# Kernel tuning notes

Hardware: AMD Instinct MI355X
Metric: run time of the kernel (lower is better)

The kernel has to match this reference:

```python
import jax, jax.numpy as jnp
import numpy as np

DIM = 1024
NUM_HEADS = 16
HEAD_DIM = DIM // NUM_HEADS
B, T = 2, 2048


def setup_inputs() -> dict:
    key = jax.random.key(0)
    ks = jax.random.split(key, 7)
    x = jax.random.normal(ks[0], (B, T, DIM), dtype=jnp.float32)
    # causal mask, broadcastable over batch and heads
    mask = jnp.tril(jnp.ones((T, T), dtype=bool))[None, None, :, :]
    # rope tables for half rotary angles, tiled to head_dim (cat of two halves)
    pos = jnp.arange(T, dtype=jnp.float32)[:, None]
    inv_freq = 1.0 / (10000.0 ** (jnp.arange(0, HEAD_DIM, 2, dtype=jnp.float32) / HEAD_DIM))
    ang = pos * inv_freq[None, :]                      # [T, hd/2]
    ang = jnp.concatenate([ang, ang], axis=-1)         # [T, hd]
    rope_sin = jnp.sin(ang)[None, None, :, :]
    rope_cos = jnp.cos(ang)[None, None, :, :]
    s = 0.02
    qkv_w = jax.random.normal(ks[1], (DIM, 3 * DIM), dtype=jnp.float32) * s
    qkv_b = jnp.zeros((3 * DIM,), dtype=jnp.float32)
    proj_w = jax.random.normal(ks[2], (DIM, DIM), dtype=jnp.float32) * s
    proj_b = jnp.zeros((DIM,), dtype=jnp.float32)
    return {"x": x, "mask": mask, "rope_sin": rope_sin, "rope_cos": rope_cos,
            "qkv_w": qkv_w, "qkv_b": qkv_b, "proj_w": proj_w, "proj_b": proj_b}


def _rotate_half(t):
    half = t.shape[-1] // 2
    return jnp.concatenate([-t[..., half:], t[..., :half]], axis=-1)


def _apply_rope(t, sin, cos):
    return t * cos + _rotate_half(t) * sin


def reference(x, mask, rope_sin, rope_cos, qkv_w, qkv_b, proj_w, proj_b):
    Bb, Tt, C = x.shape
    qkv = x @ qkv_w + qkv_b                            # [B, T, 3C]
    q, k, v = jnp.split(qkv, 3, axis=-1)
    def split_heads(t):                                # [B, T, C] -> [B, H, T, hd]
        return t.reshape(Bb, Tt, NUM_HEADS, HEAD_DIM).transpose(0, 2, 1, 3)
    q, k, v = split_heads(q), split_heads(k), split_heads(v)
    sin = rope_sin[:, :, :Tt, :]
    cos = rope_cos[:, :, :Tt, :]
    q = _apply_rope(q, sin, cos)
    k = _apply_rope(k, sin, cos)
    att = jnp.einsum("bhqd,bhkd->bhqk", q, k) / (HEAD_DIM ** 0.5)
    att = jnp.where(mask, att, -jnp.inf)
    att = jax.nn.softmax(att, axis=-1)
    y = jnp.einsum("bhqk,bhkd->bhqd", att, v)          # [B, H, T, hd]
    y = y.transpose(0, 2, 1, 3).reshape(Bb, Tt, C)
    return y @ proj_w + proj_b
```

## Files before the change

kernel.cpp:

```cpp
#include <hip/hip_runtime.h>

typedef unsigned short u16;
typedef u16 u16x8 __attribute__((ext_vector_type(8)));
typedef __bf16 bf16x8 __attribute__((ext_vector_type(8)));
typedef float f32x4 __attribute__((ext_vector_type(4)));

#define T_SEQ 2048
#define DIM 1024
#define NH 16
#define HD 64

#define MFMA(a, b, c) __builtin_amdgcn_mfma_f32_16x16x32_bf16(a, b, c, 0, 0, 0)

__device__ __forceinline__ u16 f2bf(float f) {
  return __builtin_bit_cast(u16, static_cast<__bf16>(f));
}

__device__ __forceinline__ bf16x8 ld8(const u16* p) {
  return __builtin_bit_cast(bf16x8, *(const u16x8*)p);
}

__device__ __forceinline__ void gload_lds16(const u16* g, u16* l) {
  __builtin_amdgcn_global_load_lds((const __attribute__((address_space(1))) void*)(g),
                                   (__attribute__((address_space(3))) void*)(l),
                                   16, 0, 0);
}

__global__ void k_prep(const float* __restrict__ X, u16* __restrict__ Y,
                       const float* __restrict__ Wq, u16* __restrict__ WqT,
                       const float* __restrict__ Wp, u16* __restrict__ WpT) {
  __shared__ float tile[32][33];
  int bid = blockIdx.x;
  if (bid < 4096) {
    int i = (bid * 256 + threadIdx.x) * 4;
    float4 f = *(const float4*)&X[i];
    ushort4 o = make_ushort4(f2bf(f.x), f2bf(f.y), f2bf(f.z), f2bf(f.w));
    *(ushort4*)&Y[i] = o;
    return;
  }
  const float* W; u16* WT; int K = 1024, N, bx, by;
  if (bid < 4096 + 3072) { int t = bid - 4096; W = Wq; WT = WqT; N = 3072; bx = t % 96; by = t / 96; }
  else                   { int t = bid - 7168; W = Wp; WT = WpT; N = 1024; bx = t % 32; by = t / 32; }
  int tx = threadIdx.x & 31, ty = threadIdx.x >> 5;
  int c0 = bx * 32, r0 = by * 32;
#pragma unroll
  for (int r = 0; r < 4; r++)
    tile[ty + r * 8][tx] = W[(r0 + ty + r * 8) * N + c0 + tx];
  __syncthreads();
#pragma unroll
  for (int r = 0; r < 4; r++)
    WT[(c0 + ty + r * 8) * K + r0 + tx] = f2bf(tile[tx][ty + r * 8]);
}


#define GEMM_STAGE3(buf, kk)                                                      \
  {                                                                               \
    _Pragma("unroll") for (int p = 0; p < 2; p++) {                               \
      int rr = w * 32 + p * 16;                                                   \
      gload_lds16(&Agp[(size_t)(rowBase + rr + srow) * Kd + (kk) + schunk],       \
                  &As[buf][rr * 32]);                                             \
      gload_lds16(&Bgp[(size_t)(colBase + rr + srow) * Kd + (kk) + schunk],       \
                  &Bs[buf][rr * 32]);                                             \
    }                                                                             \
  }

#define GEMM_COMPUTE3(buf)                                                        \
  {                                                                               \
    bf16x8 af[4], bfv[4];                                                         \
    _Pragma("unroll") for (int i = 0; i < 4; i++) {                               \
      af[i] = ld8(&As[buf][(wm * 64 + i * 16 + l15) * 32 + quad * 8]);            \
      bfv[i] = ld8(&Bs[buf][(wn * 64 + i * 16 + l15) * 32 + quad * 8]);           \
    }                                                                             \
    _Pragma("unroll") for (int i = 0; i < 4; i++)                                 \
        _Pragma("unroll") for (int j = 0; j < 4; j++)                             \
            acc[i][j] = MFMA(af[i], bfv[j], acc[i][j]);                           \
  }

#define GEMM_CORE3(Aptr, BTptr, bxv, byv)                                         \
  const int tid = threadIdx.x;                                                    \
  const int lane = tid & 63, w = tid >> 6;                                        \
  const int l15 = lane & 15, quad = lane >> 4;                                    \
  const int wm = w >> 1, wn = w & 1;                                              \
  const int rowBase = (byv) * 128;                                                \
  const int colBase = (bxv) * 128;                                                \
  const u16* Agp = (Aptr);                                                        \
  const u16* Bgp = (BTptr);                                                       \
  const int Kd = DIM;                                                             \
  f32x4 acc[4][4];                                                                \
  _Pragma("unroll") for (int i = 0; i < 4; i++)                                   \
      _Pragma("unroll") for (int j = 0; j < 4; j++)                               \
          acc[i][j] = (f32x4){0.f, 0.f, 0.f, 0.f};                                \
  const int srow = lane >> 2;                 \
  const int schunk = (lane & 3) * 8;    \
  GEMM_STAGE3(0, 0)                                                               \
  GEMM_STAGE3(1, 32)                                                              \
  _Pragma("unroll") for (int s = 0; s < 32; ++s) {                                \
    if (s < 31) { asm volatile("s_waitcnt vmcnt(4)" ::: "memory"); }              \
    else        { asm volatile("s_waitcnt vmcnt(0)" ::: "memory"); }              \
    __builtin_amdgcn_s_barrier();                                                 \
    if (s + 2 < 32) { GEMM_STAGE3((s + 2) % 3, (s + 2) * 32) }                    \
    GEMM_COMPUTE3(s % 3)                                                          \
  }                                                                               \
  __syncthreads();

#define EPLD 136

__global__ __launch_bounds__(256) void k_gemm_qkv(
    const u16* __restrict__ A, const u16* __restrict__ BT,
    const float* __restrict__ bias,
    const float* __restrict__ rsin, const float* __restrict__ rcos,
    u16* __restrict__ qb, u16* __restrict__ kb, u16* __restrict__ vtb) {
  __shared__ __align__(16) u16 LDSBUF[24576];
  u16 (*As)[128 * 32] = (u16(*)[128 * 32])(LDSBUF);
  u16 (*Bs)[128 * 32] = (u16(*)[128 * 32])(LDSBUF + 12288);
  const int n = blockIdx.x, xcd = n & 7, s = n >> 3;
  const int cg = xcd & 1, rg = xcd >> 1;
  const int bxv = cg * 12 + (s >> 3);
  const int byv = rg * 8 + (s & 7);
  GEMM_CORE3(A, BT, bxv, byv)

#pragma unroll
  for (int j = 0; j < 4; j++) {
    float bv = bias[colBase + wn * 64 + j * 16 + l15];
#pragma unroll
    for (int i = 0; i < 4; i++)
#pragma unroll
      for (int r = 0; r < 4; r++) acc[i][j][r] += bv;
  }

  const int colW = colBase + wn * 64;
  const int sec = colW >> 10;

  if (sec == 2) {
#pragma unroll
    for (int i = 0; i < 4; i++)
#pragma unroll
      for (int r = 0; r < 4; r++) {
        int tl = wm * 64 + i * 16 + quad * 4 + r;
#pragma unroll
        for (int j = 0; j < 4; j++) {
          int d2 = wn * 64 + j * 16 + l15;
          LDSBUF[d2 * EPLD + tl] = f2bf(acc[i][j][r]);
        }
      }
  } else {
#pragma unroll
    for (int i = 0; i < 4; i++)
#pragma unroll
      for (int r = 0; r < 4; r++) {
        int tl = wm * 64 + i * 16 + quad * 4 + r;
        int t = (rowBase + tl) & 2047;
#pragma unroll
        for (int j = 0; j < 4; j++) {
          int d = j * 16 + l15;
          float v = acc[i][j][r];
          float pr = acc[i][j ^ 2][r];
          float rot = (j < 2) ? -pr : pr;
          float rv = v * rcos[t * HD + d] + rot * rsin[t * HD + d];
          if (sec == 0) rv *= 0.125f;
          LDSBUF[tl * EPLD + wn * 64 + d] = f2bf(rv);
        }
      }
  }
  __syncthreads();

  const int hb = (colBase & 1023) >> 6;
  const int b = rowBase >> 11, t0 = rowBase & 2047;
  if (sec == 2) {
#pragma unroll
    for (int p = 0; p < 8; p++) {
      int drow = (tid >> 4) + p * 16;
      int tc = (tid & 15) * 8;
      int hh = hb + (drow >> 6), d = drow & 63;
      u16x8 v = *(const u16x8*)&LDSBUF[drow * EPLD + tc];
      *(u16x8*)&vtb[((size_t)(b * NH + hh) * HD + d) * T_SEQ + t0 + tc] = v;
    }
  } else {
    u16* dst = (sec == 0) ? qb : kb;
#pragma unroll
    for (int p = 0; p < 8; p++) {
      int row = (tid >> 4) + p * 16;
      int dc = (tid & 15) * 8;
      int hh = hb + (dc >> 6), d = dc & 63;
      u16x8 v = *(const u16x8*)&LDSBUF[row * EPLD + dc];
      *(u16x8*)&dst[((size_t)(b * NH + hh) * T_SEQ + t0 + row) * HD + d] = v;
    }
  }
}

__global__ __launch_bounds__(256) void k_gemm_proj(
    const u16* __restrict__ A, const u16* __restrict__ BT,
    const float* __restrict__ bias, float* __restrict__ C) {
  __shared__ __align__(16) u16 LDSBUF[24576];
  u16 (*As)[128 * 32] = (u16(*)[128 * 32])(LDSBUF);
  u16 (*Bs)[128 * 32] = (u16(*)[128 * 32])(LDSBUF + 12288);
  const int n = blockIdx.x, xcd = n & 7, s = n >> 3;
  const int cg = xcd & 1, rg = xcd >> 1;
  const int bxv = cg * 4 + (s >> 3);
  const int byv = rg * 8 + (s & 7);
  GEMM_CORE3(A, BT, bxv, byv)

#pragma unroll
  for (int i = 0; i < 4; i++)
#pragma unroll
    for (int r = 0; r < 4; r++) {
      int grow = rowBase + wm * 64 + i * 16 + quad * 4 + r;
#pragma unroll
      for (int j = 0; j < 4; j++) {
        int col = colBase + wn * 64 + j * 16 + l15;
        C[grow * DIM + col] = acc[i][j][r] + bias[col];
      }
    }
}

#define KLD 72
#define VLD 136

__global__ __launch_bounds__(256, 3) void k_attn(
    const u16* __restrict__ qb, const u16* __restrict__ kb,
    const u16* __restrict__ vtb, u16* __restrict__ yb) {
  __shared__ __align__(16) u16 Ks[128 * KLD];
  __shared__ __align__(16) u16 VTs[64 * VLD];
  __shared__ __align__(16) u16 Ps[64 * VLD];
  const int tid = threadIdx.x;
  const int lane = tid & 63, w = tid >> 6;
  const int l15 = lane & 15, quad = lane >> 4;
  const int bh = blockIdx.x;
  const int qt = 31 - blockIdx.y;

  const u16* qp = qb + (size_t)bh * T_SEQ * HD;
  const u16* kp = kb + (size_t)bh * T_SEQ * HD;
  const u16* vp = vtb + (size_t)bh * HD * T_SEQ;

  const int nch = (qt + 2) >> 1;
  const int qrow_base = qt * 64 + w * 16 + quad * 4;

  const int sr = tid >> 3, sc = (tid & 7) * 8;
  const int vr = tid >> 4, vc = (tid & 15) * 8;

  u16x8 kreg[4], vreg[4];
#define LOADKV(c)                                                              \
  {                                                                            \
    _Pragma("unroll") for (int p = 0; p < 4; p++)                              \
        kreg[p] = *(const u16x8*)&kp[((c) * 128 + sr + p * 32) * HD + sc];     \
    _Pragma("unroll") for (int p = 0; p < 4; p++)                              \
        vreg[p] = *(const u16x8*)&vp[(vr + p * 16) * T_SEQ + (c) * 128 + vc];  \
  }
#define WRITEK()                                                               \
  {                                                                            \
    _Pragma("unroll") for (int p = 0; p < 4; p++)                              \
        *(u16x8*)&Ks[(sr + p * 32) * KLD + sc] = kreg[p];                      \
  }
#define WRITEV()                                                               \
  {                                                                            \
    _Pragma("unroll") for (int p = 0; p < 4; p++)                              \
        *(u16x8*)&VTs[(vr + p * 16) * VLD + vc] = vreg[p];                     \
  }

  LOADKV(0)

  {
#pragma unroll
    for (int p = 0; p < 2; p++) {
      int r = sr + p * 32;
      *(u16x8*)&Ps[r * KLD + sc] = *(const u16x8*)&qp[(qt * 64 + r) * HD + sc];
    }
  }
  __syncthreads();
  bf16x8 qa0 = ld8(&Ps[(w * 16 + l15) * KLD + quad * 8]);
  bf16x8 qa1 = ld8(&Ps[(w * 16 + l15) * KLD + 32 + quad * 8]);
  WRITEK()
  WRITEV()
  __syncthreads();

  f32x4 o[4];
#pragma unroll
  for (int j = 0; j < 4; j++) o[j] = (f32x4){0.f, 0.f, 0.f, 0.f};
  float li[4] = {0.f, 0.f, 0.f, 0.f};

  u16* ps = &Ps[w * 16 * VLD];
  const int srd = ((l15 & 1) << 3) | ((l15 >> 2) << 1) | ((l15 >> 1) & 1);

  for (int c = 0; c < nch; c++) {
    const bool more = (c + 1 < nch);
    if (more) LOADKV(c + 1)

    f32x4 s[8];
#pragma unroll
    for (int j = 0; j < 8; j++) {
      s[j] = (f32x4){0.f, 0.f, 0.f, 0.f};
      bf16x8 b0 = ld8(&Ks[(j * 16 + l15) * KLD + quad * 8]);
      bf16x8 b1 = ld8(&Ks[(j * 16 + l15) * KLD + 32 + quad * 8]);
      s[j] = MFMA(qa0, b0, s[j]);
      s[j] = MFMA(qa1, b1, s[j]);
    }

    if (more) {
      asm volatile("s_waitcnt lgkmcnt(0)" ::: "memory");
      __builtin_amdgcn_s_barrier();
      __builtin_amdgcn_sched_barrier(0);
      WRITEK()
    }

    const bool lastc = (c == nch - 1);
#pragma unroll
    for (int r = 0; r < 4; r++) {
      const int swr = ((r & 1) << 3) | (quad << 1) | (r >> 1);
#pragma unroll
      for (int j = 0; j < 8; j++) {
        float e = __expf(s[j][r]);
        if (lastc && (c * 128 + j * 16 + l15 > qrow_base + r)) e = 0.f;
        li[r] += e;
        ps[swr * VLD + j * 16 + l15] = f2bf(e);
      }
    }

#pragma unroll
    for (int c4 = 0; c4 < 4; c4++) {
      bf16x8 pa = ld8(&ps[srd * VLD + c4 * 32 + quad * 8]);
#pragma unroll
      for (int j2 = 0; j2 < 4; j2++) {
        bf16x8 vb = ld8(&VTs[(j2 * 16 + l15) * VLD + c4 * 32 + quad * 8]);
        o[j2] = MFMA(pa, vb, o[j2]);
      }
    }

    if (more) {
      __syncthreads();
      WRITEV()
    }
  }

#pragma unroll
  for (int r = 0; r < 4; r++) {
#pragma unroll
    for (int off = 8; off >= 1; off >>= 1) li[r] += __shfl_xor(li[r], off, 16);
    li[r] = 1.0f / li[r];
  }

#pragma unroll
  for (int j = 0; j < 4; j++)
#pragma unroll
    for (int r = 0; r < 4; r++) {
      const int swr = ((r & 1) << 3) | (quad << 1) | (r >> 1);
      ps[swr * VLD + j * 16 + l15] = f2bf(o[j][r] * li[r]);
    }
  __syncthreads();

  const int b = bh >> 4, h = bh & 15;
  {
    int sr2 = tid >> 3, sc2 = (tid & 7) * 8;
#pragma unroll
    for (int p = 0; p < 2; p++) {
      int row = sr2 + p * 32;
      int m = row & 15;
      int srow = ((m & 1) << 3) | ((m >> 2) << 1) | ((m >> 1) & 1);
      int t = qt * 64 + row;
      *(u16x8*)&yb[((size_t)(b * T_SEQ + t) * NH + h) * HD + sc2] =
          *(const u16x8*)&Ps[((row & 48) | srow) * VLD + sc2];
    }
  }
}

extern "C" void kernel_launch(void* const* d_in, const int* in_sizes, int n_in,
                              void* d_out, int out_size, void* d_ws, size_t ws_size,
                              hipStream_t stream) {
  const float* x      = (const float*)d_in[0];
  const float* rsin   = (const float*)d_in[2];
  const float* rcos   = (const float*)d_in[3];
  const float* qkv_w  = (const float*)d_in[4];
  const float* qkv_b  = (const float*)d_in[5];
  const float* proj_w = (const float*)d_in[6];
  const float* proj_b = (const float*)d_in[7];
  float* out = (float*)d_out;

  char* ws = (char*)d_ws;
  u16* x_bf  = (u16*)(ws);
  u16* qkvT  = (u16*)(ws + (8ull << 20));
  u16* projT = (u16*)(ws + (14ull << 20));
  u16* q_buf = (u16*)(ws + (16ull << 20));
  u16* k_buf = (u16*)(ws + (24ull << 20));
  u16* vT    = (u16*)(ws + (32ull << 20));
  u16* y_buf = (u16*)(ws + (40ull << 20));

  hipLaunchKernelGGL(k_prep, dim3(8192), dim3(256), 0, stream,
                     x, x_bf, qkv_w, qkvT, proj_w, projT);
  hipLaunchKernelGGL(k_gemm_qkv, dim3(768), dim3(256), 0, stream,
                     x_bf, qkvT, qkv_b, rsin, rcos, q_buf, k_buf, vT);
  hipLaunchKernelGGL(k_attn, dim3(32, 32), dim3(256), 0, stream,
                     q_buf, k_buf, vT, y_buf);
  hipLaunchKernelGGL(k_gemm_proj, dim3(256), dim3(256), 0, stream,
                     y_buf, projT, proj_b, out);
}
```

Before: 183.3 us.

## Retile projection GEMM to 128x64 with triple-buffered LDS and use raw exp2

Measured after the change: 188.3 us. 2.7% more time.

```diff
diff --git a/kernel.cpp b/kernel.cpp
--- a/kernel.cpp
+++ b/kernel.cpp
@@ -157,7 +157,7 @@
           float pr = acc[i][j ^ 2][r];
           float rot = (j < 2) ? -pr : pr;
           float rv = v * rcos[t * HD + d] + rot * rsin[t * HD + d];
-          if (sec == 0) rv *= 0.125f;
+          if (sec == 0) rv *= 0.18033688011112042f;
           LDSBUF[tl * EPLD + wn * 64 + d] = f2bf(rv);
         }
       }
@@ -191,14 +191,57 @@
 __global__ __launch_bounds__(256) void k_gemm_proj(
     const u16* __restrict__ A, const u16* __restrict__ BT,
     const float* __restrict__ bias, float* __restrict__ C) {
-  __shared__ __align__(16) u16 LDSBUF[24576];
-  u16 (*As)[128 * 32] = (u16(*)[128 * 32])(LDSBUF);
-  u16 (*Bs)[128 * 32] = (u16(*)[128 * 32])(LDSBUF + 12288);
+  __shared__ __align__(16) u16 AsP[3][4096];
+  __shared__ __align__(16) u16 BsP[3][2048];
   const int n = blockIdx.x, xcd = n & 7, s = n >> 3;
   const int cg = xcd & 1, rg = xcd >> 1;
-  const int bxv = cg * 4 + (s >> 3);
+  const int bxv = cg * 8 + (s >> 3);
   const int byv = rg * 8 + (s & 7);
-  GEMM_CORE3(A, BT, bxv, byv)
+  const int tid = threadIdx.x;
+  const int lane = tid & 63, w = tid >> 6;
+  const int l15 = lane & 15, quad = lane >> 4;
+  const int wm = w >> 1, wn = w & 1;
+  const int rowBase = byv * 128;
+  const int colBase = bxv * 64;
+  const int srow = lane >> 2, schunk = (lane & 3) * 8;
+  f32x4 acc[4][2];
+#pragma unroll
+  for (int i = 0; i < 4; i++)
+#pragma unroll
+    for (int j = 0; j < 2; j++) acc[i][j] = (f32x4){0.f, 0.f, 0.f, 0.f};
+
+#define PROJ_STAGE(buf, kk)                                                       \
+  {                                                                               \
+    _Pragma("unroll") for (int p = 0; p < 2; p++) {                               \
+      int rr = w * 32 + p * 16;                                                   \
+      gload_lds16(&A[(size_t)(rowBase + rr + srow) * DIM + (kk) + schunk],        \
+                  &AsP[buf][rr * 32]);                                            \
+    }                                                                             \
+    gload_lds16(&BT[(size_t)(colBase + w * 16 + srow) * DIM + (kk) + schunk],     \
+                &BsP[buf][w * 16 * 32]);                                          \
+  }
+#define PROJ_COMPUTE(buf)                                                         \
+  {                                                                               \
+    bf16x8 af[4], bfv[2];                                                         \
+    _Pragma("unroll") for (int i = 0; i < 4; i++)                                 \
+        af[i] = ld8(&AsP[buf][(wm * 64 + i * 16 + l15) * 32 + quad * 8]);         \
+    _Pragma("unroll") for (int j = 0; j < 2; j++)                                 \
+        bfv[j] = ld8(&BsP[buf][(wn * 32 + j * 16 + l15) * 32 + quad * 8]);        \
+    _Pragma("unroll") for (int i = 0; i < 4; i++)                                 \
+        _Pragma("unroll") for (int j = 0; j < 2; j++)                             \
+            acc[i][j] = MFMA(af[i], bfv[j], acc[i][j]);                           \
+  }
+
+  PROJ_STAGE(0, 0)
+  PROJ_STAGE(1, 32)
+#pragma unroll
+  for (int s2 = 0; s2 < 32; ++s2) {
+    if (s2 < 31) { asm volatile("s_waitcnt vmcnt(3)" ::: "memory"); }
+    else         { asm volatile("s_waitcnt vmcnt(0)" ::: "memory"); }
+    __builtin_amdgcn_s_barrier();
+    if (s2 + 2 < 32) { PROJ_STAGE((s2 + 2) % 3, (s2 + 2) * 32) }
+    PROJ_COMPUTE(s2 % 3)
+  }
 
 #pragma unroll
   for (int i = 0; i < 4; i++)
@@ -206,8 +249,8 @@
     for (int r = 0; r < 4; r++) {
       int grow = rowBase + wm * 64 + i * 16 + quad * 4 + r;
 #pragma unroll
-      for (int j = 0; j < 4; j++) {
-        int col = colBase + wn * 64 + j * 16 + l15;
+      for (int j = 0; j < 2; j++) {
+        int col = colBase + wn * 32 + j * 16 + l15;
         C[grow * DIM + col] = acc[i][j][r] + bias[col];
       }
     }
@@ -308,7 +351,8 @@
       const int swr = ((r & 1) << 3) | (quad << 1) | (r >> 1);
 #pragma unroll
       for (int j = 0; j < 8; j++) {
-        float e = __expf(s[j][r]);
+        float e;
+        asm("v_exp_f32 %0, %1" : "=v"(e) : "v"(s[j][r]));
         if (lastc && (c * 128 + j * 16 + l15 > qrow_base + r)) e = 0.f;
         li[r] += e;
         ps[swr * VLD + j * 16 + l15] = f2bf(e);
@@ -354,10 +398,10 @@
     for (int p = 0; p < 2; p++) {
       int row = sr2 + p * 32;
       int m = row & 15;
-      int srow = ((m & 1) << 3) | ((m >> 2) << 1) | ((m >> 1) & 1);
+      int srow2 = ((m & 1) << 3) | ((m >> 2) << 1) | ((m >> 1) & 1);
       int t = qt * 64 + row;
       *(u16x8*)&yb[((size_t)(b * T_SEQ + t) * NH + h) * HD + sc2] =
-          *(const u16x8*)&Ps[((row & 48) | srow) * VLD + sc2];
+          *(const u16x8*)&Ps[((row & 48) | srow2) * VLD + sc2];
     }
   }
 }
@@ -389,6 +433,6 @@
                      x_bf, qkvT, qkv_b, rsin, rcos, q_buf, k_buf, vT);
   hipLaunchKernelGGL(k_attn, dim3(32, 32), dim3(256), 0, stream,
                      q_buf, k_buf, vT, y_buf);
-  hipLaunchKernelGGL(k_gemm_proj, dim3(256), dim3(256), 0, stream,
+  hipLaunchKernelGGL(k_gemm_proj, dim3(512), dim3(256), 0, stream,
                      y_buf, projT, proj_b, out);
 }
```
